# Performance work log

Measured on AMD Instinct MI355X. Metric: run time of the kernel, lower is better.

## Reference

```python
import jax, jax.numpy as jnp
import numpy as np

DIM = 128
N = 16384
N_USERS = 512
SAME_USER_BIAS = 5.0

def setup_inputs() -> dict:
    key = jax.random.key(0)
    kx, ku, kq, kk, kv = jax.random.split(key, 5)
    x = jax.random.normal(kx, (N, DIM), dtype=jnp.float32)
    user_ids = jax.random.randint(ku, (N,), 0, N_USERS, dtype=jnp.int64)
    s = 1.0 / np.sqrt(DIM)
    Wq = jax.random.normal(kq, (DIM, DIM), dtype=jnp.float32) * s
    Wk = jax.random.normal(kk, (DIM, DIM), dtype=jnp.float32) * s
    Wv = jax.random.normal(kv, (DIM, DIM), dtype=jnp.float32) * s
    return {"x": x, "user_ids": user_ids, "Wq": Wq, "Wk": Wk, "Wv": Wv}

def reference(x, user_ids, Wq, Wk, Wv):
    # nn.Linear(dim, dim, bias=False): y = x @ W.T
    Q = x @ Wq.T  # [N, d]
    K = x @ Wk.T
    V = x @ Wv.T
    scale = jnp.asarray(DIM ** 0.5, dtype=x.dtype)
    logits = (Q @ K.T) / scale  # [N, N]
    S = (user_ids[:, None] == user_ids[None, :]).astype(logits.dtype)
    logits = logits + SAME_USER_BIAS * S
    A = jax.nn.softmax(logits, axis=1)
    return A @ V
```

## Files before the change

kernel.cpp:

```cpp
#include <hip/hip_runtime.h>
#include <hip/hip_bf16.h>

#define N_TOK 16384
#define DIM   128
#define JT     64

#define KROW 128
#define VROW 64
#define PROW 32

using bf16x8 = __attribute__((ext_vector_type(8))) short;
using f32x4  = __attribute__((ext_vector_type(4))) float;

static __device__ __forceinline__ unsigned short f2b(float f) {
    union { __hip_bfloat16 h; unsigned short u; } cv;
    cv.h = __float2bfloat16(f);
    return cv.u;
}

static __device__ __forceinline__ bf16x8 load8f(const float* p) {
    float4 a = *reinterpret_cast<const float4*>(p);
    float4 b = *reinterpret_cast<const float4*>(p + 4);
    bf16x8 r;
    r[0] = (short)f2b(a.x); r[1] = (short)f2b(a.y);
    r[2] = (short)f2b(a.z); r[3] = (short)f2b(a.w);
    r[4] = (short)f2b(b.x); r[5] = (short)f2b(b.y);
    r[6] = (short)f2b(b.z); r[7] = (short)f2b(b.w);
    return r;
}

__global__ __launch_bounds__(256)
void marker_kernel(float* out, float val)
{
    int i = blockIdx.x * 256 + threadIdx.x;
    if (i < N_TOK * DIM) out[i] = val;
}

__global__ __launch_bounds__(256)
void qkv_kernel(const float* __restrict__ x,
                const float* __restrict__ wq,
                const float* __restrict__ wk,
                const float* __restrict__ wv,
                unsigned short* __restrict__ Q,
                unsigned short* __restrict__ K,
                unsigned short* __restrict__ Vt)
{
    const int t = threadIdx.x;
    const int wave = t >> 6, lane = t & 63;
    const int ln = lane & 15, quad = lane >> 4, q8 = quad * 8;
    const int z = blockIdx.y;
    const float* W = (z == 0) ? wq : (z == 1) ? wk : wv;
    const int r0 = blockIdx.x * 64 + wave * 16;

    bf16x8 a[4];
#pragma unroll
    for (int ks = 0; ks < 4; ++ks)
        a[ks] = load8f(&x[(size_t)(r0 + ln) * DIM + ks * 32 + q8]);

    f32x4 acc[8];
#pragma unroll
    for (int nt = 0; nt < 8; ++nt) acc[nt] = f32x4{0.f, 0.f, 0.f, 0.f};

#pragma unroll
    for (int nt = 0; nt < 8; ++nt)
#pragma unroll
        for (int ks = 0; ks < 4; ++ks) {
            bf16x8 b = load8f(&W[(size_t)(nt * 16 + ln) * DIM + ks * 32 + q8]);
            acc[nt] = __builtin_amdgcn_mfma_f32_16x16x32_bf16(a[ks], b, acc[nt], 0, 0, 0);
        }

#pragma unroll
    for (int nt = 0; nt < 8; ++nt) {
        const int col = nt * 16 + ln;
        if (z == 2) {
            ushort4 v4;
            v4.x = f2b(acc[nt][0]); v4.y = f2b(acc[nt][1]);
            v4.z = f2b(acc[nt][2]); v4.w = f2b(acc[nt][3]);
            *reinterpret_cast<ushort4*>(&Vt[(size_t)col * N_TOK + r0 + quad * 4]) = v4;
        } else {
            unsigned short* dst = (z == 0) ? Q : K;
#pragma unroll
            for (int r = 0; r < 4; ++r)
                dst[(size_t)(r0 + quad * 4 + r) * DIM + col] = f2b(acc[nt][r]);
        }
    }
}

__global__ __launch_bounds__(256, 2)
void flash_kernel(const unsigned short* __restrict__ Q,
                  const unsigned short* __restrict__ K,
                  const unsigned short* __restrict__ Vt,
                  const unsigned int* __restrict__ u32,
                  int jspan,
                  float* __restrict__ pO, float* __restrict__ pl,
                  float* __restrict__ out)
{
    __shared__ unsigned short kb[2][JT * KROW];
    __shared__ unsigned short vb[2][DIM * VROW];
    __shared__ unsigned short pbuf[4][32 * PROW];
    __shared__ int ub[2][JT];

    const int t = threadIdx.x;
    const int wave = t >> 6, lane = t & 63;
    const int ln = lane & 15, quad = lane >> 4, q8 = quad * 8;
    const int r0 = blockIdx.x * 128 + wave * 32;
    const int split = blockIdx.y;
    const int j0 = split * jspan;
    const int j1 = j0 + jspan;

    const float lscale = 1.4426950408889634f * 0.08838834764831845f;
    const float cbias  = 5.0f * 1.4426950408889634f - 16.0f;
    const float cnob   = -16.0f;

    bool i64 = true;
    for (int k = 0; k < 64; ++k) i64 = i64 && (u32[2 * k + 1] == 0u);

    bf16x8 qf[2][4];
    int uq[2][4];
#pragma unroll
    for (int mt = 0; mt < 2; ++mt) {
#pragma unroll
        for (int ks = 0; ks < 4; ++ks)
            qf[mt][ks] = *reinterpret_cast<const bf16x8*>(
                &Q[(size_t)(r0 + mt * 16 + ln) * DIM + ks * 32 + q8]);
#pragma unroll
        for (int r = 0; r < 4; ++r) {
            int i = r0 + mt * 16 + quad * 4 + r;
            uq[mt][r] = (int)(i64 ? u32[2 * i] : u32[i]);
        }
    }

    f32x4 o[2][8];
#pragma unroll
    for (int mt = 0; mt < 2; ++mt)
#pragma unroll
        for (int dt = 0; dt < 8; ++dt) o[mt][dt] = f32x4{0.f, 0.f, 0.f, 0.f};
    float lsum[2][4];
#pragma unroll
    for (int mt = 0; mt < 2; ++mt)
#pragma unroll
        for (int r = 0; r < 4; ++r) lsum[mt][r] = 0.f;

    unsigned short* pw = &pbuf[wave][0];

    {
#pragma unroll
        for (int p = 0; p < 4; ++p) {
            int slot = p * 256 + t;
            int row = slot >> 4, seg = slot & 15;
            int ss = seg ^ (row & 7);
            *reinterpret_cast<uint4*>(&kb[0][row * KROW + ss * 8]) =
                *reinterpret_cast<const uint4*>(&K[(size_t)(j0 + row) * DIM + seg * 8]);
        }
#pragma unroll
        for (int p = 0; p < 4; ++p) {
            int slot = p * 256 + t;
            int row = slot >> 3, seg = slot & 7;
            int ss = seg ^ (row & 7);
            *reinterpret_cast<uint4*>(&vb[0][row * VROW + ss * 8]) =
                *reinterpret_cast<const uint4*>(&Vt[(size_t)row * N_TOK + j0 + seg * 8]);
        }
        if (t < JT) {
            int i = j0 + t;
            ub[0][t] = (int)(i64 ? u32[2 * i] : u32[i]);
        }
    }
    __syncthreads();

    int c = 0;
    for (int j = j0; j < j1; j += JT) {
        int jn = j + JT;
        if (jn >= j1) jn = j0;

        uint4 kreg[4];
#pragma unroll
        for (int p = 0; p < 4; ++p) {
            int slot = p * 256 + t;
            int row = slot >> 4, seg = slot & 15;
            kreg[p] = *reinterpret_cast<const uint4*>(&K[(size_t)(jn + row) * DIM + seg * 8]);
        }
        uint4 vreg[4];
#pragma unroll
        for (int p = 0; p < 4; ++p) {
            int slot = p * 256 + t;
            int row = slot >> 3, seg = slot & 7;
            vreg[p] = *reinterpret_cast<const uint4*>(&Vt[(size_t)row * N_TOK + jn + seg * 8]);
        }
        int ureg = 0;
        if (t < JT) ureg = (int)(i64 ? u32[2 * (jn + t)] : u32[jn + t]);

        f32x4 s[2][4];
#pragma unroll
        for (int mt = 0; mt < 2; ++mt)
#pragma unroll
            for (int nt = 0; nt < 4; ++nt) s[mt][nt] = f32x4{0.f, 0.f, 0.f, 0.f};
        __builtin_amdgcn_s_setprio(1);
#pragma unroll
        for (int nt = 0; nt < 4; ++nt)
#pragma unroll
            for (int ks = 0; ks < 4; ++ks) {
                int row = nt * 16 + ln;
                int sc = (ks * 4 + quad) ^ (row & 7);
                bf16x8 b = *reinterpret_cast<const bf16x8*>(&kb[c][row * KROW + sc * 8]);
                s[0][nt] = __builtin_amdgcn_mfma_f32_16x16x32_bf16(qf[0][ks], b, s[0][nt], 0, 0, 0);
                s[1][nt] = __builtin_amdgcn_mfma_f32_16x16x32_bf16(qf[1][ks], b, s[1][nt], 0, 0, 0);
            }
        __builtin_amdgcn_s_setprio(0);

        int uk[4];
#pragma unroll
        for (int nt = 0; nt < 4; ++nt) uk[nt] = ub[c][nt * 16 + ln];

#pragma unroll
        for (int k2 = 0; k2 < 2; ++k2) {
#pragma unroll
            for (int mt = 0; mt < 2; ++mt)
#pragma unroll
                for (int r = 0; r < 4; ++r) {
                    int row = mt * 16 + quad * 4 + r;
                    int rx = (row >> 1) & 3;
#pragma unroll
                    for (int nh = 0; nh < 2; ++nh) {
                        int nt = k2 * 2 + nh;
                        float v = s[mt][nt][r] * lscale + (uq[mt][r] == uk[nt] ? cbias : cnob);
                        float p = exp2f(v);
                        lsum[mt][r] += p;
                        int lc = nh * 16 + ln;
                        pw[row * PROW + (((lc >> 3) ^ rx) << 3) + (lc & 7)] = f2b(p);
                    }
                }

            bf16x8 pa[2];
#pragma unroll
            for (int mt = 0; mt < 2; ++mt) {
                int row = mt * 16 + ln;
                int sc = quad ^ ((row >> 1) & 3);
                pa[mt] = *reinterpret_cast<const bf16x8*>(&pw[row * PROW + sc * 8]);
            }

            __builtin_amdgcn_s_setprio(1);
#pragma unroll
            for (int dt = 0; dt < 8; ++dt) {
                int row = dt * 16 + ln;
                int sc = (k2 * 4 + quad) ^ (row & 7);
                bf16x8 b = *reinterpret_cast<const bf16x8*>(&vb[c][row * VROW + sc * 8]);
                o[0][dt] = __builtin_amdgcn_mfma_f32_16x16x32_bf16(pa[0], b, o[0][dt], 0, 0, 0);
                o[1][dt] = __builtin_amdgcn_mfma_f32_16x16x32_bf16(pa[1], b, o[1][dt], 0, 0, 0);
            }
            __builtin_amdgcn_s_setprio(0);
        }

#pragma unroll
        for (int p = 0; p < 4; ++p) {
            int slot = p * 256 + t;
            int row = slot >> 4, seg = slot & 15;
            int ss = seg ^ (row & 7);
            *reinterpret_cast<uint4*>(&kb[c ^ 1][row * KROW + ss * 8]) = kreg[p];
        }
#pragma unroll
        for (int p = 0; p < 4; ++p) {
            int slot = p * 256 + t;
            int row = slot >> 3, seg = slot & 7;
            int ss = seg ^ (row & 7);
            *reinterpret_cast<uint4*>(&vb[c ^ 1][row * VROW + ss * 8]) = vreg[p];
        }
        if (t < JT) ub[c ^ 1][t] = ureg;

        __syncthreads();
        c ^= 1;
    }

#pragma unroll
    for (int mt = 0; mt < 2; ++mt)
#pragma unroll
        for (int r = 0; r < 4; ++r) {
            float l = lsum[mt][r];
            l += __shfl_xor(l, 1, 64);
            l += __shfl_xor(l, 2, 64);
            l += __shfl_xor(l, 4, 64);
            l += __shfl_xor(l, 8, 64);
            lsum[mt][r] = l;
        }

    if (out != nullptr) {
#pragma unroll
        for (int mt = 0; mt < 2; ++mt)
#pragma unroll
            for (int r = 0; r < 4; ++r) {
                float l = lsum[mt][r];
                bool lbad = !(l > 0.f) || !(l < 3.0e38f);
                float inv = 1.0f / l;
                int row = r0 + mt * 16 + quad * 4 + r;
#pragma unroll
                for (int dt = 0; dt < 8; ++dt) {
                    float v = o[mt][dt][r] * inv;
                    if (v != v) v = 12345.0f;
                    if (lbad)   v = 23456.0f;
                    out[(size_t)row * DIM + dt * 16 + ln] = v;
                }
            }
    } else {
        const size_t base = (size_t)split * N_TOK;
#pragma unroll
        for (int mt = 0; mt < 2; ++mt) {
#pragma unroll
            for (int r = 0; r < 4; ++r) {
                int row = r0 + mt * 16 + quad * 4 + r;
#pragma unroll
                for (int dt = 0; dt < 8; ++dt)
                    pO[(base + row) * DIM + dt * 16 + ln] = o[mt][dt][r];
                if (ln == 0)
                    pl[base + row] = lsum[mt][r];
            }
        }
    }
}

__global__ __launch_bounds__(256)
void merge_kernel(const float* __restrict__ pO, const float* __restrict__ pl,
                  float* __restrict__ out, int ns)
{
    const int t = threadIdx.x;
    const int wave = t >> 6, lane = t & 63;
    const int row = blockIdx.x * 4 + wave;
    const int c = lane * 2;

    float l = 0.f;
    for (int s = 0; s < ns; ++s) l += pl[(size_t)s * N_TOK + row];
    bool lbad = !(l > 0.f) || !(l < 3.0e38f);
    float inv = 1.0f / l;

    float a0 = 0.f, a1 = 0.f;
    for (int s = 0; s < ns; ++s) {
        const float2 v = *reinterpret_cast<const float2*>(
            &pO[((size_t)s * N_TOK + row) * DIM + c]);
        a0 += v.x; a1 += v.y;
    }
    float v0 = a0 * inv, v1 = a1 * inv;
    if (v0 != v0) v0 = 12345.0f;
    if (v1 != v1) v1 = 12345.0f;
    if (lbad) { v0 = 23456.0f; v1 = 23456.0f; }
    float2 res; res.x = v0; res.y = v1;
    *reinterpret_cast<float2*>(&out[(size_t)row * DIM + c]) = res;
}

extern "C" void kernel_launch(void* const* d_in, const int* in_sizes, int n_in,
                              void* d_out, int out_size, void* d_ws, size_t ws_size,
                              hipStream_t stream)
{
    float* out = (float*)d_out;

    bool ok = (n_in == 5) &&
              in_sizes[0] == N_TOK * DIM && in_sizes[1] == N_TOK &&
              in_sizes[2] == DIM * DIM && in_sizes[3] == DIM * DIM &&
              in_sizes[4] == DIM * DIM && out_size == N_TOK * DIM;
    if (!ok) { marker_kernel<<<8192, 256, 0, stream>>>(out, 5555.f); return; }

    const float*        xf  = (const float*)d_in[0];
    const unsigned int* u32 = (const unsigned int*)d_in[1];
    const float*        wqf = (const float*)d_in[2];
    const float*        wkf = (const float*)d_in[3];
    const float*        wvf = (const float*)d_in[4];

    char* ws = (char*)d_ws;
    size_t off = 0;
    unsigned short* Q  = (unsigned short*)(ws + off); off += (size_t)N_TOK * DIM * 2;
    unsigned short* K  = (unsigned short*)(ws + off); off += (size_t)N_TOK * DIM * 2;
    unsigned short* Vt = (unsigned short*)(ws + off); off += (size_t)N_TOK * DIM * 2;

    if (ws_size < off) { marker_kernel<<<8192, 256, 0, stream>>>(out, 4444.f); return; }

    const size_t per_split = (size_t)N_TOK * DIM * 4 + (size_t)N_TOK * 4;
    int nsplit = 1;
    if (ws_size >= off + 4 * per_split)      nsplit = 4;
    else if (ws_size >= off + 2 * per_split) nsplit = 2;

    qkv_kernel<<<dim3(N_TOK / 64, 3), 256, 0, stream>>>(xf, wqf, wkf, wvf, Q, K, Vt);

    if (nsplit >= 2) {
        float* pO = (float*)(ws + off);
        float* pl = (float*)(ws + off + (size_t)nsplit * N_TOK * DIM * 4);
        flash_kernel<<<dim3(N_TOK / 128, nsplit), 256, 0, stream>>>(
            Q, K, Vt, u32, N_TOK / nsplit, pO, pl, nullptr);
        merge_kernel<<<N_TOK / 4, 256, 0, stream>>>(pO, pl, out, nsplit);
    } else {
        flash_kernel<<<dim3(N_TOK / 128, 1), 256, 0, stream>>>(
            Q, K, Vt, u32, N_TOK, nullptr, nullptr, out);
    }
}
```

Baseline: 303.2 us.

## Use 8 waves of 16 query rows per flash block instead of 4 waves of 32

The flash kernel now runs 512 threads per block, and each wave owns 16 query rows instead of 32. This halves the per-wave registers for Q fragments, S and O accumulators, and the K/V prefetch loads are spread across twice as many threads. The aim is higher occupancy and better latency hiding. In exchange, every K and V fragment read from LDS now feeds only one MFMA instead of two, which doubles LDS read traffic per FLOP and lowers MFMA-to-load reuse.

```diff
diff --git a/kernel.cpp b/kernel.cpp
--- a/kernel.cpp
+++ b/kernel.cpp
@@ -86,7 +86,7 @@
     }
 }
 
-__global__ __launch_bounds__(256, 2)
+__global__ __launch_bounds__(512, 4)
 void flash_kernel(const unsigned short* __restrict__ Q,
                   const unsigned short* __restrict__ K,
                   const unsigned short* __restrict__ Vt,
@@ -97,13 +97,13 @@
 {
     __shared__ unsigned short kb[2][JT * KROW];
     __shared__ unsigned short vb[2][DIM * VROW];
-    __shared__ unsigned short pbuf[4][32 * PROW];
+    __shared__ unsigned short pbuf[8][16 * PROW];
     __shared__ int ub[2][JT];
 
     const int t = threadIdx.x;
     const int wave = t >> 6, lane = t & 63;
     const int ln = lane & 15, quad = lane >> 4, q8 = quad * 8;
-    const int r0 = blockIdx.x * 128 + wave * 32;
+    const int r0 = blockIdx.x * 128 + wave * 16;
     const int split = blockIdx.y;
     const int j0 = split * jspan;
     const int j1 = j0 + jspan;
@@ -115,46 +115,39 @@
     bool i64 = true;
     for (int k = 0; k < 64; ++k) i64 = i64 && (u32[2 * k + 1] == 0u);
 
-    bf16x8 qf[2][4];
-    int uq[2][4];
-#pragma unroll
-    for (int mt = 0; mt < 2; ++mt) {
-#pragma unroll
-        for (int ks = 0; ks < 4; ++ks)
-            qf[mt][ks] = *reinterpret_cast<const bf16x8*>(
-                &Q[(size_t)(r0 + mt * 16 + ln) * DIM + ks * 32 + q8]);
-#pragma unroll
-        for (int r = 0; r < 4; ++r) {
-            int i = r0 + mt * 16 + quad * 4 + r;
-            uq[mt][r] = (int)(i64 ? u32[2 * i] : u32[i]);
-        }
-    }
-
-    f32x4 o[2][8];
-#pragma unroll
-    for (int mt = 0; mt < 2; ++mt)
-#pragma unroll
-        for (int dt = 0; dt < 8; ++dt) o[mt][dt] = f32x4{0.f, 0.f, 0.f, 0.f};
-    float lsum[2][4];
-#pragma unroll
-    for (int mt = 0; mt < 2; ++mt)
-#pragma unroll
-        for (int r = 0; r < 4; ++r) lsum[mt][r] = 0.f;
+    bf16x8 qf[4];
+    int uq[4];
+#pragma unroll
+    for (int ks = 0; ks < 4; ++ks)
+        qf[ks] = *reinterpret_cast<const bf16x8*>(
+            &Q[(size_t)(r0 + ln) * DIM + ks * 32 + q8]);
+#pragma unroll
+    for (int r = 0; r < 4; ++r) {
+        int i = r0 + quad * 4 + r;
+        uq[r] = (int)(i64 ? u32[2 * i] : u32[i]);
+    }
+
+    f32x4 o[8];
+#pragma unroll
+    for (int dt = 0; dt < 8; ++dt) o[dt] = f32x4{0.f, 0.f, 0.f, 0.f};
+    float lsum[4];
+#pragma unroll
+    for (int r = 0; r < 4; ++r) lsum[r] = 0.f;
 
     unsigned short* pw = &pbuf[wave][0];
 
     {
 #pragma unroll
-        for (int p = 0; p < 4; ++p) {
-            int slot = p * 256 + t;
+        for (int p = 0; p < 2; ++p) {
+            int slot = p * 512 + t;
             int row = slot >> 4, seg = slot & 15;
             int ss = seg ^ (row & 7);
             *reinterpret_cast<uint4*>(&kb[0][row * KROW + ss * 8]) =
                 *reinterpret_cast<const uint4*>(&K[(size_t)(j0 + row) * DIM + seg * 8]);
         }
 #pragma unroll
-        for (int p = 0; p < 4; ++p) {
-            int slot = p * 256 + t;
+        for (int p = 0; p < 2; ++p) {
+            int slot = p * 512 + t;
             int row = slot >> 3, seg = slot & 7;
             int ss = seg ^ (row & 7);
             *reinterpret_cast<uint4*>(&vb[0][row * VROW + ss * 8]) =
@@ -172,28 +165,26 @@
         int jn = j + JT;
         if (jn >= j1) jn = j0;
 
-        uint4 kreg[4];
-#pragma unroll
-        for (int p = 0; p < 4; ++p) {
-            int slot = p * 256 + t;
+        uint4 kreg[2];
+#pragma unroll
+        for (int p = 0; p < 2; ++p) {
+            int slot = p * 512 + t;
             int row = slot >> 4, seg = slot & 15;
             kreg[p] = *reinterpret_cast<const uint4*>(&K[(size_t)(jn + row) * DIM + seg * 8]);
         }
-        uint4 vreg[4];
-#pragma unroll
-        for (int p = 0; p < 4; ++p) {
-            int slot = p * 256 + t;
+        uint4 vreg[2];
+#pragma unroll
+        for (int p = 0; p < 2; ++p) {
+            int slot = p * 512 + t;
             int row = slot >> 3, seg = slot & 7;
             vreg[p] = *reinterpret_cast<const uint4*>(&Vt[(size_t)row * N_TOK + jn + seg * 8]);
         }
         int ureg = 0;
         if (t < JT) ureg = (int)(i64 ? u32[2 * (jn + t)] : u32[jn + t]);
 
-        f32x4 s[2][4];
-#pragma unroll
-        for (int mt = 0; mt < 2; ++mt)
-#pragma unroll
-            for (int nt = 0; nt < 4; ++nt) s[mt][nt] = f32x4{0.f, 0.f, 0.f, 0.f};
+        f32x4 s[4];
+#pragma unroll
+        for (int nt = 0; nt < 4; ++nt) s[nt] = f32x4{0.f, 0.f, 0.f, 0.f};
         __builtin_amdgcn_s_setprio(1);
 #pragma unroll
         for (int nt = 0; nt < 4; ++nt)
@@ -202,8 +193,7 @@
                 int row = nt * 16 + ln;
                 int sc = (ks * 4 + quad) ^ (row & 7);
                 bf16x8 b = *reinterpret_cast<const bf16x8*>(&kb[c][row * KROW + sc * 8]);
-                s[0][nt] = __builtin_amdgcn_mfma_f32_16x16x32_bf16(qf[0][ks], b, s[0][nt], 0, 0, 0);
-                s[1][nt] = __builtin_amdgcn_mfma_f32_16x16x32_bf16(qf[1][ks], b, s[1][nt], 0, 0, 0);
+                s[nt] = __builtin_amdgcn_mfma_f32_16x16x32_bf16(qf[ks], b, s[nt], 0, 0, 0);
             }
         __builtin_amdgcn_s_setprio(0);
 
@@ -214,28 +204,25 @@
 #pragma unroll
         for (int k2 = 0; k2 < 2; ++k2) {
 #pragma unroll
-            for (int mt = 0; mt < 2; ++mt)
-#pragma unroll
-                for (int r = 0; r < 4; ++r) {
-                    int row = mt * 16 + quad * 4 + r;
-                    int rx = (row >> 1) & 3;
-#pragma unroll
-                    for (int nh = 0; nh < 2; ++nh) {
-                        int nt = k2 * 2 + nh;
-                        float v = s[mt][nt][r] * lscale + (uq[mt][r] == uk[nt] ? cbias : cnob);
-                        float p = exp2f(v);
-                        lsum[mt][r] += p;
-                        int lc = nh * 16 + ln;
-                        pw[row * PROW + (((lc >> 3) ^ rx) << 3) + (lc & 7)] = f2b(p);
-                    }
+            for (int r = 0; r < 4; ++r) {
+                int row = quad * 4 + r;
+                int rx = (row >> 1) & 3;
+#pragma unroll
+                for (int nh = 0; nh < 2; ++nh) {
+                    int nt = k2 * 2 + nh;
+                    float v = s[nt][r] * lscale + (uq[r] == uk[nt] ? cbias : cnob);
+                    float p = exp2f(v);
+                    lsum[r] += p;
+                    int lc = nh * 16 + ln;
+                    pw[row * PROW + (((lc >> 3) ^ rx) << 3) + (lc & 7)] = f2b(p);
                 }
-
-            bf16x8 pa[2];
-#pragma unroll
-            for (int mt = 0; mt < 2; ++mt) {
-                int row = mt * 16 + ln;
+            }
+
+            bf16x8 pa;
+            {
+                int row = ln;
                 int sc = quad ^ ((row >> 1) & 3);
-                pa[mt] = *reinterpret_cast<const bf16x8*>(&pw[row * PROW + sc * 8]);
+                pa = *reinterpret_cast<const bf16x8*>(&pw[row * PROW + sc * 8]);
             }
 
             __builtin_amdgcn_s_setprio(1);
@@ -244,22 +231,21 @@
                 int row = dt * 16 + ln;
                 int sc = (k2 * 4 + quad) ^ (row & 7);
                 bf16x8 b = *reinterpret_cast<const bf16x8*>(&vb[c][row * VROW + sc * 8]);
-                o[0][dt] = __builtin_amdgcn_mfma_f32_16x16x32_bf16(pa[0], b, o[0][dt], 0, 0, 0);
-                o[1][dt] = __builtin_amdgcn_mfma_f32_16x16x32_bf16(pa[1], b, o[1][dt], 0, 0, 0);
+                o[dt] = __builtin_amdgcn_mfma_f32_16x16x32_bf16(pa, b, o[dt], 0, 0, 0);
             }
             __builtin_amdgcn_s_setprio(0);
         }
 
 #pragma unroll
-        for (int p = 0; p < 4; ++p) {
-            int slot = p * 256 + t;
+        for (int p = 0; p < 2; ++p) {
+            int slot = p * 512 + t;
             int row = slot >> 4, seg = slot & 15;
             int ss = seg ^ (row & 7);
             *reinterpret_cast<uint4*>(&kb[c ^ 1][row * KROW + ss * 8]) = kreg[p];
         }
 #pragma unroll
-        for (int p = 0; p < 4; ++p) {
-            int slot = p * 256 + t;
+        for (int p = 0; p < 2; ++p) {
+            int slot = p * 512 + t;
             int row = slot >> 3, seg = slot & 7;
             int ss = seg ^ (row & 7);
             *reinterpret_cast<uint4*>(&vb[c ^ 1][row * VROW + ss * 8]) = vreg[p];
@@ -271,47 +257,40 @@
     }
 
 #pragma unroll
-    for (int mt = 0; mt < 2; ++mt)
+    for (int r = 0; r < 4; ++r) {
+        float l = lsum[r];
+        l += __shfl_xor(l, 1, 64);
+        l += __shfl_xor(l, 2, 64);
+        l += __shfl_xor(l, 4, 64);
+        l += __shfl_xor(l, 8, 64);
+        lsum[r] = l;
+    }
+
+    if (out != nullptr) {
 #pragma unroll
         for (int r = 0; r < 4; ++r) {
-            float l = lsum[mt][r];
-            l += __shfl_xor(l, 1, 64);
-            l += __shfl_xor(l, 2, 64);
-            l += __shfl_xor(l, 4, 64);
-            l += __shfl_xor(l, 8, 64);
-            lsum[mt][r] = l;
-        }
-
-    if (out != nullptr) {
-#pragma unroll
-        for (int mt = 0; mt < 2; ++mt)
-#pragma unroll
-            for (int r = 0; r < 4; ++r) {
-                float l = lsum[mt][r];
-                bool lbad = !(l > 0.f) || !(l < 3.0e38f);
-                float inv = 1.0f / l;
-                int row = r0 + mt * 16 + quad * 4 + r;
-#pragma unroll
-                for (int dt = 0; dt < 8; ++dt) {
-                    float v = o[mt][dt][r] * inv;
-                    if (v != v) v = 12345.0f;
-                    if (lbad)   v = 23456.0f;
-                    out[(size_t)row * DIM + dt * 16 + ln] = v;
-                }
-            }
+            float l = lsum[r];
+            bool lbad = !(l > 0.f) || !(l < 3.0e38f);
+            float inv = 1.0f / l;
+            int row = r0 + quad * 4 + r;
+#pragma unroll
+            for (int dt = 0; dt < 8; ++dt) {
+                float v = o[dt][r] * inv;
+                if (v != v) v = 12345.0f;
+                if (lbad)   v = 23456.0f;
+                out[(size_t)row * DIM + dt * 16 + ln] = v;
+            }
+        }
     } else {
         const size_t base = (size_t)split * N_TOK;
 #pragma unroll
-        for (int mt = 0; mt < 2; ++mt) {
-#pragma unroll
-            for (int r = 0; r < 4; ++r) {
-                int row = r0 + mt * 16 + quad * 4 + r;
-#pragma unroll
-                for (int dt = 0; dt < 8; ++dt)
-                    pO[(base + row) * DIM + dt * 16 + ln] = o[mt][dt][r];
-                if (ln == 0)
-                    pl[base + row] = lsum[mt][r];
-            }
+        for (int r = 0; r < 4; ++r) {
+            int row = r0 + quad * 4 + r;
+#pragma unroll
+            for (int dt = 0; dt < 8; ++dt)
+                pO[(base + row) * DIM + dt * 16 + ln] = o[dt][r];
+            if (ln == 0)
+                pl[base + row] = lsum[r];
         }
     }
 }
@@ -380,11 +359,11 @@
     if (nsplit >= 2) {
         float* pO = (float*)(ws + off);
         float* pl = (float*)(ws + off + (size_t)nsplit * N_TOK * DIM * 4);
-        flash_kernel<<<dim3(N_TOK / 128, nsplit), 256, 0, stream>>>(
+        flash_kernel<<<dim3(N_TOK / 128, nsplit), 512, 0, stream>>>(
             Q, K, Vt, u32, N_TOK / nsplit, pO, pl, nullptr);
         merge_kernel<<<N_TOK / 4, 256, 0, stream>>>(pO, pl, out, nsplit);
     } else {
-        flash_kernel<<<dim3(N_TOK / 128, 1), 256, 0, stream>>>(
+        flash_kernel<<<dim3(N_TOK / 128, 1), 512, 0, stream>>>(
             Q, K, Vt, u32, N_TOK, nullptr, nullptr, out);
     }
 }
```

Measured after the change: 315.3 us. +4.0%, slower.

## Switch attention to 32x32x16 MFMA with transposed S and register-resident P

Applied to the files above, without the earlier changes.

Rewrites the flash kernel's inner loop to use 32x32x16 bf16 MFMAs. It computes S transposed (K as the A operand, Q as B) so each lane holds one query row's scores. The probabilities are packed to bf16 and rearranged across lane halves with shuffles, replacing the per-wave LDS staging buffer for P and its write/read round trip. Row sums become a single scalar per lane, and the final normalisation goes through a small LDS buffer. The V-tile LDS store is moved after the PV MFMAs to overlap with compute. The risk is higher register pressure from 16-wide accumulators, which could hurt occupancy at two blocks per CU.

```diff
diff --git a/kernel.cpp b/kernel.cpp
--- a/kernel.cpp
+++ b/kernel.cpp
@@ -7,10 +7,11 @@
 
 #define KROW 128
 #define VROW 64
-#define PROW 32
-
-using bf16x8 = __attribute__((ext_vector_type(8))) short;
-using f32x4  = __attribute__((ext_vector_type(4))) float;
+
+using bf16x8 = __attribute__((ext_vector_type(8)))  short;
+using f32x4  = __attribute__((ext_vector_type(4)))  float;
+using f32x16 = __attribute__((ext_vector_type(16))) float;
+using i32x4  = __attribute__((ext_vector_type(4)))  int;
 
 static __device__ __forceinline__ unsigned short f2b(float f) {
     union { __hip_bfloat16 h; unsigned short u; } cv;
@@ -95,15 +96,15 @@
                   float* __restrict__ pO, float* __restrict__ pl,
                   float* __restrict__ out)
 {
-    __shared__ unsigned short kb[2][JT * KROW];
-    __shared__ unsigned short vb[2][DIM * VROW];
-    __shared__ unsigned short pbuf[4][32 * PROW];
-    __shared__ int ub[2][JT];
+    __shared__ __align__(16) unsigned short kb[2][JT * KROW];
+    __shared__ __align__(16) unsigned short vb[2][DIM * VROW];
+    __shared__ __align__(16) int   ub[2][JT];
+    __shared__ __align__(16) float lbuf[4][32];
 
     const int t = threadIdx.x;
     const int wave = t >> 6, lane = t & 63;
-    const int ln = lane & 15, quad = lane >> 4, q8 = quad * 8;
-    const int r0 = blockIdx.x * 128 + wave * 32;
+    const int q31 = lane & 31, hi = lane >> 5;
+    const int r0w = blockIdx.x * 128 + wave * 32;
     const int split = blockIdx.y;
     const int j0 = split * jspan;
     const int j1 = j0 + jspan;
@@ -115,33 +116,20 @@
     bool i64 = true;
     for (int k = 0; k < 64; ++k) i64 = i64 && (u32[2 * k + 1] == 0u);
 
-    bf16x8 qf[2][4];
-    int uq[2][4];
-#pragma unroll
-    for (int mt = 0; mt < 2; ++mt) {
-#pragma unroll
-        for (int ks = 0; ks < 4; ++ks)
-            qf[mt][ks] = *reinterpret_cast<const bf16x8*>(
-                &Q[(size_t)(r0 + mt * 16 + ln) * DIM + ks * 32 + q8]);
-#pragma unroll
-        for (int r = 0; r < 4; ++r) {
-            int i = r0 + mt * 16 + quad * 4 + r;
-            uq[mt][r] = (int)(i64 ? u32[2 * i] : u32[i]);
-        }
-    }
-
-    f32x4 o[2][8];
-#pragma unroll
-    for (int mt = 0; mt < 2; ++mt)
-#pragma unroll
-        for (int dt = 0; dt < 8; ++dt) o[mt][dt] = f32x4{0.f, 0.f, 0.f, 0.f};
-    float lsum[2][4];
-#pragma unroll
-    for (int mt = 0; mt < 2; ++mt)
-#pragma unroll
-        for (int r = 0; r < 4; ++r) lsum[mt][r] = 0.f;
-
-    unsigned short* pw = &pbuf[wave][0];
+    bf16x8 qf[8];
+#pragma unroll
+    for (int dt = 0; dt < 8; ++dt)
+        qf[dt] = *reinterpret_cast<const bf16x8*>(
+            &Q[(size_t)(r0w + q31) * DIM + dt * 16 + hi * 8]);
+
+    const int uq = (int)(i64 ? u32[2 * (r0w + q31)] : u32[r0w + q31]);
+
+    f32x16 o[4];
+#pragma unroll
+    for (int nt = 0; nt < 4; ++nt)
+#pragma unroll
+        for (int r = 0; r < 16; ++r) o[nt][r] = 0.f;
+    float lsum = 0.f;
 
     {
 #pragma unroll
@@ -189,65 +177,63 @@
         int ureg = 0;
         if (t < JT) ureg = (int)(i64 ? u32[2 * (jn + t)] : u32[jn + t]);
 
-        f32x4 s[2][4];
-#pragma unroll
-        for (int mt = 0; mt < 2; ++mt)
-#pragma unroll
-            for (int nt = 0; nt < 4; ++nt) s[mt][nt] = f32x4{0.f, 0.f, 0.f, 0.f};
+        f32x16 s0v, s1v;
+#pragma unroll
+        for (int r = 0; r < 16; ++r) { s0v[r] = 0.f; s1v[r] = 0.f; }
         __builtin_amdgcn_s_setprio(1);
 #pragma unroll
-        for (int nt = 0; nt < 4; ++nt)
-#pragma unroll
-            for (int ks = 0; ks < 4; ++ks) {
-                int row = nt * 16 + ln;
-                int sc = (ks * 4 + quad) ^ (row & 7);
-                bf16x8 b = *reinterpret_cast<const bf16x8*>(&kb[c][row * KROW + sc * 8]);
-                s[0][nt] = __builtin_amdgcn_mfma_f32_16x16x32_bf16(qf[0][ks], b, s[0][nt], 0, 0, 0);
-                s[1][nt] = __builtin_amdgcn_mfma_f32_16x16x32_bf16(qf[1][ks], b, s[1][nt], 0, 0, 0);
+        for (int dt = 0; dt < 8; ++dt) {
+            int seg = (dt * 2 + hi) ^ (q31 & 7);
+            bf16x8 k0 = *reinterpret_cast<const bf16x8*>(&kb[c][q31 * KROW + seg * 8]);
+            bf16x8 k1 = *reinterpret_cast<const bf16x8*>(&kb[c][(32 + q31) * KROW + seg * 8]);
+            s0v = __builtin_amdgcn_mfma_f32_32x32x16_bf16(k0, qf[dt], s0v, 0, 0, 0);
+            s1v = __builtin_amdgcn_mfma_f32_32x32x16_bf16(k1, qf[dt], s1v, 0, 0, 0);
+        }
+        __builtin_amdgcn_s_setprio(0);
+
+        bf16x8 pa[4];
+#pragma unroll
+        for (int kv32 = 0; kv32 < 2; ++kv32) {
+            i32x4 ukg[4];
+#pragma unroll
+            for (int g = 0; g < 4; ++g)
+                ukg[g] = *reinterpret_cast<const i32x4*>(&ub[c][32 * kv32 + 8 * g + 4 * hi]);
+
+            unsigned int dw[4][2];
+#pragma unroll
+            for (int g = 0; g < 4; ++g) {
+                float p0, p1, p2, p3;
+                {
+                    float v0 = __builtin_fmaf((kv32 ? s1v : s0v)[4 * g + 0], lscale,
+                                              (uq == ukg[g][0]) ? cbias : cnob);
+                    float v1 = __builtin_fmaf((kv32 ? s1v : s0v)[4 * g + 1], lscale,
+                                              (uq == ukg[g][1]) ? cbias : cnob);
+                    float v2 = __builtin_fmaf((kv32 ? s1v : s0v)[4 * g + 2], lscale,
+                                              (uq == ukg[g][2]) ? cbias : cnob);
+                    float v3 = __builtin_fmaf((kv32 ? s1v : s0v)[4 * g + 3], lscale,
+                                              (uq == ukg[g][3]) ? cbias : cnob);
+                    p0 = exp2f(v0); p1 = exp2f(v1); p2 = exp2f(v2); p3 = exp2f(v3);
+                }
+                lsum += (p0 + p1) + (p2 + p3);
+                dw[g][0] = (unsigned int)f2b(p0) | ((unsigned int)f2b(p1) << 16);
+                dw[g][1] = (unsigned int)f2b(p2) | ((unsigned int)f2b(p3) << 16);
             }
-        __builtin_amdgcn_s_setprio(0);
-
-        int uk[4];
-#pragma unroll
-        for (int nt = 0; nt < 4; ++nt) uk[nt] = ub[c][nt * 16 + ln];
-
-#pragma unroll
-        for (int k2 = 0; k2 < 2; ++k2) {
-#pragma unroll
-            for (int mt = 0; mt < 2; ++mt)
-#pragma unroll
-                for (int r = 0; r < 4; ++r) {
-                    int row = mt * 16 + quad * 4 + r;
-                    int rx = (row >> 1) & 3;
-#pragma unroll
-                    for (int nh = 0; nh < 2; ++nh) {
-                        int nt = k2 * 2 + nh;
-                        float v = s[mt][nt][r] * lscale + (uq[mt][r] == uk[nt] ? cbias : cnob);
-                        float p = exp2f(v);
-                        lsum[mt][r] += p;
-                        int lc = nh * 16 + ln;
-                        pw[row * PROW + (((lc >> 3) ^ rx) << 3) + (lc & 7)] = f2b(p);
-                    }
-                }
-
-            bf16x8 pa[2];
-#pragma unroll
-            for (int mt = 0; mt < 2; ++mt) {
-                int row = mt * 16 + ln;
-                int sc = quad ^ ((row >> 1) & 3);
-                pa[mt] = *reinterpret_cast<const bf16x8*>(&pw[row * PROW + sc * 8]);
+
+#pragma unroll
+            for (int kt = 0; kt < 2; ++kt) {
+                unsigned int s0d = hi ? dw[2 * kt][0] : dw[2 * kt + 1][0];
+                unsigned int s1d = hi ? dw[2 * kt][1] : dw[2 * kt + 1][1];
+                unsigned int r0d = (unsigned int)__shfl_xor((int)s0d, 32, 64);
+                unsigned int r1d = (unsigned int)__shfl_xor((int)s1d, 32, 64);
+                unsigned int k0d = hi ? dw[2 * kt + 1][0] : dw[2 * kt][0];
+                unsigned int k1d = hi ? dw[2 * kt + 1][1] : dw[2 * kt][1];
+                union { unsigned int u[4]; bf16x8 v; } pu;
+                pu.u[0] = hi ? r0d : k0d;
+                pu.u[1] = hi ? r1d : k1d;
+                pu.u[2] = hi ? k0d : r0d;
+                pu.u[3] = hi ? k1d : r1d;
+                pa[kv32 * 2 + kt] = pu.v;
             }
-
-            __builtin_amdgcn_s_setprio(1);
-#pragma unroll
-            for (int dt = 0; dt < 8; ++dt) {
-                int row = dt * 16 + ln;
-                int sc = (k2 * 4 + quad) ^ (row & 7);
-                bf16x8 b = *reinterpret_cast<const bf16x8*>(&vb[c][row * VROW + sc * 8]);
-                o[0][dt] = __builtin_amdgcn_mfma_f32_16x16x32_bf16(pa[0], b, o[0][dt], 0, 0, 0);
-                o[1][dt] = __builtin_amdgcn_mfma_f32_16x16x32_bf16(pa[1], b, o[1][dt], 0, 0, 0);
-            }
-            __builtin_amdgcn_s_setprio(0);
         }
 
 #pragma unroll
@@ -257,6 +243,21 @@
             int ss = seg ^ (row & 7);
             *reinterpret_cast<uint4*>(&kb[c ^ 1][row * KROW + ss * 8]) = kreg[p];
         }
+        if (t < JT) ub[c ^ 1][t] = ureg;
+
+        __builtin_amdgcn_s_setprio(1);
+#pragma unroll
+        for (int nt = 0; nt < 4; ++nt) {
+            int row = nt * 32 + q31;
+#pragma unroll
+            for (int ktg = 0; ktg < 4; ++ktg) {
+                int seg = (ktg * 2 + hi) ^ (q31 & 7);
+                bf16x8 b = *reinterpret_cast<const bf16x8*>(&vb[c][row * VROW + seg * 8]);
+                o[nt] = __builtin_amdgcn_mfma_f32_32x32x16_bf16(pa[ktg], b, o[nt], 0, 0, 0);
+            }
+        }
+        __builtin_amdgcn_s_setprio(0);
+
 #pragma unroll
         for (int p = 0; p < 4; ++p) {
             int slot = p * 256 + t;
@@ -264,55 +265,47 @@
             int ss = seg ^ (row & 7);
             *reinterpret_cast<uint4*>(&vb[c ^ 1][row * VROW + ss * 8]) = vreg[p];
         }
-        if (t < JT) ub[c ^ 1][t] = ureg;
 
         __syncthreads();
         c ^= 1;
     }
 
-#pragma unroll
-    for (int mt = 0; mt < 2; ++mt)
-#pragma unroll
-        for (int r = 0; r < 4; ++r) {
-            float l = lsum[mt][r];
-            l += __shfl_xor(l, 1, 64);
-            l += __shfl_xor(l, 2, 64);
-            l += __shfl_xor(l, 4, 64);
-            l += __shfl_xor(l, 8, 64);
-            lsum[mt][r] = l;
-        }
+    lsum += __shfl_xor(lsum, 32, 64);
 
     if (out != nullptr) {
-#pragma unroll
-        for (int mt = 0; mt < 2; ++mt)
-#pragma unroll
-            for (int r = 0; r < 4; ++r) {
-                float l = lsum[mt][r];
-                bool lbad = !(l > 0.f) || !(l < 3.0e38f);
-                float inv = 1.0f / l;
-                int row = r0 + mt * 16 + quad * 4 + r;
-#pragma unroll
-                for (int dt = 0; dt < 8; ++dt) {
-                    float v = o[mt][dt][r] * inv;
+        bool lbad = !(lsum > 0.f) || !(lsum < 3.0e38f);
+        float inv = 1.0f / lsum;
+        if (hi == 0) lbuf[wave][q31] = lbad ? -1.0f : inv;
+        __syncthreads();
+        f32x4 ivg[4];
+#pragma unroll
+        for (int g = 0; g < 4; ++g)
+            ivg[g] = *reinterpret_cast<const f32x4*>(&lbuf[wave][8 * g + 4 * hi]);
+#pragma unroll
+        for (int nt = 0; nt < 4; ++nt)
+#pragma unroll
+            for (int g = 0; g < 4; ++g)
+#pragma unroll
+                for (int i = 0; i < 4; ++i) {
+                    int row = r0w + 8 * g + 4 * hi + i;
+                    float iv = ivg[g][i];
+                    float v = o[nt][4 * g + i] * iv;
                     if (v != v) v = 12345.0f;
-                    if (lbad)   v = 23456.0f;
-                    out[(size_t)row * DIM + dt * 16 + ln] = v;
+                    if (iv < 0.f) v = 23456.0f;
+                    out[(size_t)row * DIM + nt * 32 + q31] = v;
                 }
-            }
     } else {
         const size_t base = (size_t)split * N_TOK;
-#pragma unroll
-        for (int mt = 0; mt < 2; ++mt) {
-#pragma unroll
-            for (int r = 0; r < 4; ++r) {
-                int row = r0 + mt * 16 + quad * 4 + r;
-#pragma unroll
-                for (int dt = 0; dt < 8; ++dt)
-                    pO[(base + row) * DIM + dt * 16 + ln] = o[mt][dt][r];
-                if (ln == 0)
-                    pl[base + row] = lsum[mt][r];
-            }
-        }
+        if (hi == 0) pl[base + r0w + q31] = lsum;
+#pragma unroll
+        for (int nt = 0; nt < 4; ++nt)
+#pragma unroll
+            for (int g = 0; g < 4; ++g)
+#pragma unroll
+                for (int i = 0; i < 4; ++i) {
+                    int row = r0w + 8 * g + 4 * hi + i;
+                    pO[(base + row) * DIM + nt * 32 + q31] = o[nt][4 * g + i];
+                }
     }
 }
 
```

New measurement: 291.1 us. -4.0%, faster.
